# Optimization experiments

Hardware: AMD Instinct MI355X
Metric: run time of the kernel (lower is better)

Reference implementation:

```python
import jax, jax.numpy as jnp
import numpy as np

N, F, E = 2048, 512, 32  # batch, n_features (attention length), embedding_dim


def setup_inputs() -> dict:
    key = jax.random.key(0)
    ks = jax.random.split(key, 8)
    xav = np.sqrt(2.0 / (F + E))  # xavier_normal std for [F, E] params
    X = jax.random.normal(ks[0], (N, F), dtype=jnp.float32)
    Xi = jax.random.randint(ks[1], (N,), 0, 2).astype(jnp.float32)
    idx = jax.random.randint(ks[2], (N,), 0, F)
    I = jax.nn.one_hot(idx, F, dtype=jnp.float32)  # one-hot feature selector
    S = (jax.random.uniform(ks[3], (N, F)) < 0.5).astype(jnp.float32)
    S = S.at[:, 0].set(1.0)  # guarantee non-empty context per row
    return {
        "X": X, "Xi": Xi, "I": I, "S": S,
        "xi_w": jax.random.normal(ks[4], (F, E), jnp.float32) * xav,
        "xi_b": jax.random.normal(ks[5], (F, E), jnp.float32) * xav,
        "xs_w": jax.random.normal(ks[6], (F, E), jnp.float32) * xav,
        "xs_b": jax.random.normal(ks[7], (F, E), jnp.float32) * xav,
    }


def stable_softmax(x):
    # softmax along last dim; rows that are entirely -inf produce zeros
    m = jnp.max(x, axis=-1, keepdims=True)
    m = jnp.where(jnp.isfinite(m), m, jnp.zeros_like(m))
    e = jnp.exp(x - m)
    s = jnp.sum(e, axis=-1, keepdims=True)
    return e / jnp.maximum(s, jnp.asarray(1e-9, x.dtype))


def reference(X, Xi, I, S, xi_w, xi_b, xs_w, xs_b):
    # --- map_xs (attention aggregator) ---
    # FX: [N, F, E]; note the original reuses xs_featurizer_bias for the I-term
    FX = X[:, :, None] * xs_w[None] + xs_b[None] + (I @ xs_b)[:, None, :]
    keep = (S[:, :, None] * S[:, None, :]) > 0  # [N, F, F]
    mask = jnp.where(keep, 0.0, -jnp.inf).astype(FX.dtype)
    scale = jnp.asarray(1.0 / np.sqrt(E), FX.dtype)
    scores = mask + jnp.einsum('nqe,nke->nqk', FX * scale, FX)
    attn = stable_softmax(scores)  # [N, F, F]
    Fxs = jnp.einsum('nqk,nke->nqe', attn, FX).sum(axis=1) / S.sum(axis=1)[:, None]  # [N, E]
    # --- map_xi ---
    Iw = I @ xi_w  # [N, E]
    Ib = I @ xi_b  # [N, E]
    Fxi = Xi[:, None] * Iw + Ib
    # --- score / logz / logprob (binary, exp score) ---
    ulogp = jnp.log(jnp.exp(jnp.sum(Fxi * Fxs, axis=-1)))
    s0 = jnp.exp(jnp.sum(Ib * Fxs, axis=-1))          # Xi = 0
    s1 = jnp.exp(jnp.sum((Iw + Ib) * Fxs, axis=-1))   # Xi = 1
    logz = jnp.log(s0 + s1)
    return ulogp - logz  # [N]
```

## Files before the change

### kernel.cpp

```cpp
#include <hip/hip_runtime.h>
#include <math.h>

#define FF 512
#define EE 32
#define RS 40
#define FCAP 416
#define NTCAP 26

typedef __attribute__((ext_vector_type(8))) short bf16x8;
typedef __attribute__((ext_vector_type(4))) float f32x4;

#define SFOLD 0.5050092f

__device__ __forceinline__ unsigned short f2bf(float x) {
    unsigned int u = __float_as_uint(x);
    return (unsigned short)((u + 0x7fffu + ((u >> 16) & 1u)) >> 16);
}
__device__ __forceinline__ float bf2f(unsigned short h) {
    return __uint_as_float(((unsigned int)h) << 16);
}
__device__ __forceinline__ float esum4(f32x4 d) {
    return (__builtin_amdgcn_exp2f(d[0]) + __builtin_amdgcn_exp2f(d[1])) +
           (__builtin_amdgcn_exp2f(d[2]) + __builtin_amdgcn_exp2f(d[3]));
}

template <int NC>
__device__ __forceinline__ void pass1_cols(const unsigned short* __restrict__ myrow,
                                           float* __restrict__ Zs,
                                           int c0, int nt, int cnt, float pad, int lane) {
    bf16x8 bf[NC];
#pragma unroll
    for (int c = 0; c < NC; ++c)
        bf[c] = *(const bf16x8*)(myrow + (size_t)(c0 + c) * 16 * RS);
    float zA[NC], zB[NC];
#pragma unroll
    for (int c = 0; c < NC; ++c) { zA[c] = 0.f; zB[c] = 0.f; }
    const unsigned short* ap = myrow;
    int i = 0;
    for (; i + 2 <= nt; i += 2) {
        bf16x8 a0 = *(const bf16x8*)(ap);
        bf16x8 a1 = *(const bf16x8*)(ap + 16 * RS);
        ap += 32 * RS;
#pragma unroll
        for (int c = 0; c < NC; ++c) {
            f32x4 d0 = {0.f, 0.f, 0.f, 0.f};
            f32x4 d1 = {0.f, 0.f, 0.f, 0.f};
            d0 = __builtin_amdgcn_mfma_f32_16x16x32_bf16(a0, bf[c], d0, 0, 0, 0);
            d1 = __builtin_amdgcn_mfma_f32_16x16x32_bf16(a1, bf[c], d1, 0, 0, 0);
            zA[c] += esum4(d0);
            zB[c] += esum4(d1);
        }
    }
    if (i < nt) {
        bf16x8 a0 = *(const bf16x8*)(ap);
#pragma unroll
        for (int c = 0; c < NC; ++c) {
            f32x4 d0 = {0.f, 0.f, 0.f, 0.f};
            d0 = __builtin_amdgcn_mfma_f32_16x16x32_bf16(a0, bf[c], d0, 0, 0, 0);
            zA[c] += esum4(d0);
        }
    }
#pragma unroll
    for (int c = 0; c < NC; ++c) {
        float z = zA[c] + zB[c];
        z += __shfl_xor(z, 16);
        z += __shfl_xor(z, 32);
        if (lane < 16) {
            int q = (c0 + c) * 16 + lane;
            Zs[q] = (q < cnt) ? 1.f / fmaxf(z - pad, 1e-9f) : 0.f;
        }
    }
}

template <int NC>
__device__ __forceinline__ void pass2_cols(const unsigned short* __restrict__ myrow,
                                           const float* __restrict__ Zs,
                                           float* __restrict__ ws,
                                           int c0, int nt, int lane, int grp) {
    bf16x8 bf[NC];
#pragma unroll
    for (int c = 0; c < NC; ++c)
        bf[c] = *(const bf16x8*)(myrow + (size_t)(c0 + c) * 16 * RS);
    float wA[NC], wB[NC];
#pragma unroll
    for (int c = 0; c < NC; ++c) { wA[c] = 0.f; wB[c] = 0.f; }
    const unsigned short* ap = myrow;
    const float* zp = Zs + grp * 4;
    int i = 0;
    for (; i + 2 <= nt; i += 2) {
        bf16x8 a0 = *(const bf16x8*)(ap);
        bf16x8 a1 = *(const bf16x8*)(ap + 16 * RS);
        ap += 32 * RS;
        float4 z0 = *(const float4*)(zp);
        float4 z1 = *(const float4*)(zp + 16);
        zp += 32;
#pragma unroll
        for (int c = 0; c < NC; ++c) {
            f32x4 d0 = {0.f, 0.f, 0.f, 0.f};
            f32x4 d1 = {0.f, 0.f, 0.f, 0.f};
            d0 = __builtin_amdgcn_mfma_f32_16x16x32_bf16(a0, bf[c], d0, 0, 0, 0);
            d1 = __builtin_amdgcn_mfma_f32_16x16x32_bf16(a1, bf[c], d1, 0, 0, 0);
            float a = wA[c], b = wB[c];
            a = fmaf(__builtin_amdgcn_exp2f(d0[0]), z0.x, a);
            a = fmaf(__builtin_amdgcn_exp2f(d0[1]), z0.y, a);
            a = fmaf(__builtin_amdgcn_exp2f(d0[2]), z0.z, a);
            a = fmaf(__builtin_amdgcn_exp2f(d0[3]), z0.w, a);
            b = fmaf(__builtin_amdgcn_exp2f(d1[0]), z1.x, b);
            b = fmaf(__builtin_amdgcn_exp2f(d1[1]), z1.y, b);
            b = fmaf(__builtin_amdgcn_exp2f(d1[2]), z1.z, b);
            b = fmaf(__builtin_amdgcn_exp2f(d1[3]), z1.w, b);
            wA[c] = a; wB[c] = b;
        }
    }
    if (i < nt) {
        bf16x8 a0 = *(const bf16x8*)(ap);
        float4 z0 = *(const float4*)(zp);
#pragma unroll
        for (int c = 0; c < NC; ++c) {
            f32x4 d0 = {0.f, 0.f, 0.f, 0.f};
            d0 = __builtin_amdgcn_mfma_f32_16x16x32_bf16(a0, bf[c], d0, 0, 0, 0);
            float a = wA[c];
            a = fmaf(__builtin_amdgcn_exp2f(d0[0]), z0.x, a);
            a = fmaf(__builtin_amdgcn_exp2f(d0[1]), z0.y, a);
            a = fmaf(__builtin_amdgcn_exp2f(d0[2]), z0.z, a);
            a = fmaf(__builtin_amdgcn_exp2f(d0[3]), z0.w, a);
            wA[c] = a;
        }
    }
#pragma unroll
    for (int c = 0; c < NC; ++c) {
        float w = wA[c] + wB[c];
        w += __shfl_xor(w, 16);
        w += __shfl_xor(w, 32);
        if (lane < 16) ws[(c0 + c) * 16 + lane] = w;
    }
}

extern "C" __global__ void __launch_bounds__(512, 8)
model_kernel(const float* __restrict__ X, const float* __restrict__ Xi,
             const float* __restrict__ I, const float* __restrict__ S,
             const float* __restrict__ xi_w, const float* __restrict__ xi_b,
             const float* __restrict__ xs_w, const float* __restrict__ xs_b,
             float* __restrict__ out) {
    const int n = blockIdx.x;
    const int tid = threadIdx.x;
    const int lane = tid & 63;
    const int wv = tid >> 6;
    const int l15 = lane & 15;
    const int grp = lane >> 4;

    __shared__ __align__(16) unsigned short fxb[FCAP * RS];
    __shared__ unsigned short lst[FF];
    __shared__ __align__(16) float Zs[FCAP];
    __shared__ float ws[FCAP];
    __shared__ __align__(16) float idxb[EE];
    __shared__ float pf[16][EE];
    __shared__ float fxs_sh[EE];
    __shared__ int sh_idx;
    __shared__ int wbase[8];

    const float* Srow = S + (size_t)n * FF;
    const float* Irow = I + (size_t)n * FF;
    const float* Xrow = X + (size_t)n * FF;

    if (Irow[tid] > 0.5f) sh_idx = tid;
    bool act = Srow[tid] > 0.f;
    unsigned long long m = __ballot(act);
    int nb = __popcll(m & ((1ull << lane) - 1ull));
    if (lane == 0) wbase[wv] = __popcll(m);
    __syncthreads();

    int off = 0;
    for (int i = 0; i < wv; ++i) off += wbase[i];
    if (act) lst[off + nb] = (unsigned short)tid;
    int cntr = 0;
#pragma unroll
    for (int i = 0; i < 8; ++i) cntr += wbase[i];
    const int cnt = (cntr < FCAP) ? cntr : FCAP;
    int nt0 = (cnt + 15) >> 4;
    const int nt = (nt0 < NTCAP) ? nt0 : NTCAP;
    const int ntp16 = nt * 16;
    const int jend = ((nt + 1) >> 1) * 32;
    const int idx = sh_idx;
    if (tid < EE) idxb[tid] = xs_b[idx * EE + tid];
    __syncthreads();

    for (int jb = 0; jb < jend; jb += 64) {
        int j = jb + (tid >> 3);
        int e4 = (tid & 7) * 4;
        if (j < jend) {
            unsigned short h0 = 0, h1 = 0, h2 = 0, h3 = 0;
            if (j < cnt) {
                int f = lst[j];
                float xv = Xrow[f];
                float4 w4 = *(const float4*)(xs_w + f * EE + e4);
                float4 b4 = *(const float4*)(xs_b + f * EE + e4);
                float4 i4 = *(const float4*)(idxb + e4);
                h0 = f2bf(SFOLD * fmaf(xv, w4.x, b4.x + i4.x));
                h1 = f2bf(SFOLD * fmaf(xv, w4.y, b4.y + i4.y));
                h2 = f2bf(SFOLD * fmaf(xv, w4.z, b4.z + i4.z));
                h3 = f2bf(SFOLD * fmaf(xv, w4.w, b4.w + i4.w));
            }
            ushort4 pk = make_ushort4(h0, h1, h2, h3);
            *(ushort4*)(fxb + j * RS + e4) = pk;
        }
    }
    __syncthreads();

    const unsigned short* myrow = fxb + (size_t)l15 * RS + grp * 8;
    const float pad = (float)(ntp16 - cnt);

    const int cbase = nt >> 3, crem = nt & 7;
    const int ncols = cbase + (wv < crem ? 1 : 0);
    const int c0 = wv * cbase + (wv < crem ? wv : crem);

    switch (ncols) {
        case 1: pass1_cols<1>(myrow, Zs, c0, nt, cnt, pad, lane); break;
        case 2: pass1_cols<2>(myrow, Zs, c0, nt, cnt, pad, lane); break;
        case 3: pass1_cols<3>(myrow, Zs, c0, nt, cnt, pad, lane); break;
        case 4: pass1_cols<4>(myrow, Zs, c0, nt, cnt, pad, lane); break;
        default: break;
    }
    __syncthreads();

    switch (ncols) {
        case 1: pass2_cols<1>(myrow, Zs, ws, c0, nt, lane, grp); break;
        case 2: pass2_cols<2>(myrow, Zs, ws, c0, nt, lane, grp); break;
        case 3: pass2_cols<3>(myrow, Zs, ws, c0, nt, lane, grp); break;
        case 4: pass2_cols<4>(myrow, Zs, ws, c0, nt, lane, grp); break;
        default: break;
    }
    __syncthreads();

    {
        int e = tid & 31, g = tid >> 5;
        float acc = 0.f;
        for (int k = g; k < cnt; k += 16)
            acc += ws[k] * bf2f(fxb[k * RS + e]);
        pf[g][e] = acc;
    }
    __syncthreads();
    if (tid < EE) {
        float s = 0.f;
#pragma unroll
        for (int g = 0; g < 16; ++g) s += pf[g][tid];
        fxs_sh[tid] = s * (1.0f / SFOLD) / (float)cnt;
    }
    __syncthreads();
    if (tid < EE) {
        float fv = fxs_sh[tid];
        pf[0][tid] = xi_w[idx * EE + tid] * fv;
    }
    __syncthreads();
    if (tid == 0) {
        float a = 0.f;
#pragma unroll
        for (int e = 0; e < EE; ++e) a += pf[0][e];
        float xiv = Xi[n];
        float mm = fmaxf(a, 0.f);
        float sp = mm + logf(__expf(a - mm) + __expf(-mm));
        out[n] = xiv * a - sp;
    }
}

extern "C" void kernel_launch(void* const* d_in, const int* in_sizes, int n_in,
                              void* d_out, int out_size, void* d_ws, size_t ws_size,
                              hipStream_t stream) {
    const float* X    = (const float*)d_in[0];
    const float* Xi   = (const float*)d_in[1];
    const float* I    = (const float*)d_in[2];
    const float* S    = (const float*)d_in[3];
    const float* xi_w = (const float*)d_in[4];
    const float* xi_b = (const float*)d_in[5];
    const float* xs_w = (const float*)d_in[6];
    const float* xs_b = (const float*)d_in[7];
    float* out = (float*)d_out;
    const int N = in_sizes[1];
    hipLaunchKernelGGL(model_kernel, dim3(N), dim3(512), 0, stream,
                       X, Xi, I, S, xi_w, xi_b, xs_w, xs_b, out);
}
```

Measured before the change: 116.0 us.

## Split remainder column tiles across all waves to balance attention passes

When the number of 16-row tiles is 17 or 18, each wave takes two column tiles and the one or two leftover columns are split by row-pair ranges across all eight waves. Partial softmax denominators and weights are combined with shared-memory atomics, and the leftover denominators are inverted after a barrier. This removes the imbalance where a single wave handled a third column and set the critical path. It costs an extra barrier, atomics, and extra registers for the split-column operands.

```diff
diff --git a/kernel.cpp b/kernel.cpp
--- a/kernel.cpp
+++ b/kernel.cpp
@@ -23,21 +23,40 @@
     return (__builtin_amdgcn_exp2f(d[0]) + __builtin_amdgcn_exp2f(d[1])) +
            (__builtin_amdgcn_exp2f(d[2]) + __builtin_amdgcn_exp2f(d[3]));
 }
-
-template <int NC>
-__device__ __forceinline__ void pass1_cols(const unsigned short* __restrict__ myrow,
-                                           float* __restrict__ Zs,
-                                           int c0, int nt, int cnt, float pad, int lane) {
+__device__ __forceinline__ float wsum4(f32x4 d, float4 z, float acc) {
+    acc = fmaf(__builtin_amdgcn_exp2f(d[0]), z.x, acc);
+    acc = fmaf(__builtin_amdgcn_exp2f(d[1]), z.y, acc);
+    acc = fmaf(__builtin_amdgcn_exp2f(d[2]), z.z, acc);
+    acc = fmaf(__builtin_amdgcn_exp2f(d[3]), z.w, acc);
+    return acc;
+}
+
+template <int NC, int R>
+__device__ __forceinline__ void pass1_t(const unsigned short* __restrict__ myrow,
+                                        float* __restrict__ Zs,
+                                        int c0, int nt, int cnt, float pad,
+                                        int lane, int wv) {
     bf16x8 bf[NC];
 #pragma unroll
     for (int c = 0; c < NC; ++c)
         bf[c] = *(const bf16x8*)(myrow + (size_t)(c0 + c) * 16 * RS);
+    bf16x8 bs[R > 0 ? R : 1];
+    float sA[R > 0 ? R : 1], sB[R > 0 ? R : 1];
+    if (R > 0) {
+#pragma unroll
+        for (int s = 0; s < R; ++s) {
+            bs[s] = *(const bf16x8*)(myrow + (size_t)(nt - R + s) * 16 * RS);
+            sA[s] = 0.f; sB[s] = 0.f;
+        }
+    }
     float zA[NC], zB[NC];
 #pragma unroll
     for (int c = 0; c < NC; ++c) { zA[c] = 0.f; zB[c] = 0.f; }
+    const int NPf = nt >> 1;
+    const int NP = NPf + (nt & 1);
+    const int plo = (wv * NP) >> 3, phi = ((wv + 1) * NP) >> 3;
     const unsigned short* ap = myrow;
-    int i = 0;
-    for (; i + 2 <= nt; i += 2) {
+    for (int p = 0; p < NPf; ++p) {
         bf16x8 a0 = *(const bf16x8*)(ap);
         bf16x8 a1 = *(const bf16x8*)(ap + 16 * RS);
         ap += 32 * RS;
@@ -50,14 +69,33 @@
             zA[c] += esum4(d0);
             zB[c] += esum4(d1);
         }
-    }
-    if (i < nt) {
+        if (R > 0 && p >= plo && p < phi) {
+#pragma unroll
+            for (int s = 0; s < R; ++s) {
+                f32x4 d0 = {0.f, 0.f, 0.f, 0.f};
+                f32x4 d1 = {0.f, 0.f, 0.f, 0.f};
+                d0 = __builtin_amdgcn_mfma_f32_16x16x32_bf16(a0, bs[s], d0, 0, 0, 0);
+                d1 = __builtin_amdgcn_mfma_f32_16x16x32_bf16(a1, bs[s], d1, 0, 0, 0);
+                sA[s] += esum4(d0);
+                sB[s] += esum4(d1);
+            }
+        }
+    }
+    if (nt & 1) {
         bf16x8 a0 = *(const bf16x8*)(ap);
 #pragma unroll
         for (int c = 0; c < NC; ++c) {
             f32x4 d0 = {0.f, 0.f, 0.f, 0.f};
             d0 = __builtin_amdgcn_mfma_f32_16x16x32_bf16(a0, bf[c], d0, 0, 0, 0);
             zA[c] += esum4(d0);
+        }
+        if (R > 0 && NPf >= plo && NPf < phi) {
+#pragma unroll
+            for (int s = 0; s < R; ++s) {
+                f32x4 d0 = {0.f, 0.f, 0.f, 0.f};
+                d0 = __builtin_amdgcn_mfma_f32_16x16x32_bf16(a0, bs[s], d0, 0, 0, 0);
+                sA[s] += esum4(d0);
+            }
         }
     }
 #pragma unroll
@@ -70,24 +108,44 @@
             Zs[q] = (q < cnt) ? 1.f / fmaxf(z - pad, 1e-9f) : 0.f;
         }
     }
-}
-
-template <int NC>
-__device__ __forceinline__ void pass2_cols(const unsigned short* __restrict__ myrow,
-                                           const float* __restrict__ Zs,
-                                           float* __restrict__ ws,
-                                           int c0, int nt, int lane, int grp) {
+    if (R > 0) {
+#pragma unroll
+        for (int s = 0; s < R; ++s) {
+            float z = sA[s] + sB[s];
+            z += __shfl_xor(z, 16);
+            z += __shfl_xor(z, 32);
+            if (lane < 16) atomicAdd(&Zs[(nt - R + s) * 16 + lane], z);
+        }
+    }
+}
+
+template <int NC, int R>
+__device__ __forceinline__ void pass2_t(const unsigned short* __restrict__ myrow,
+                                        const float* __restrict__ Zs,
+                                        float* __restrict__ ws,
+                                        int c0, int nt, int lane, int grp, int wv) {
     bf16x8 bf[NC];
 #pragma unroll
     for (int c = 0; c < NC; ++c)
         bf[c] = *(const bf16x8*)(myrow + (size_t)(c0 + c) * 16 * RS);
+    bf16x8 bs[R > 0 ? R : 1];
+    float sA[R > 0 ? R : 1], sB[R > 0 ? R : 1];
+    if (R > 0) {
+#pragma unroll
+        for (int s = 0; s < R; ++s) {
+            bs[s] = *(const bf16x8*)(myrow + (size_t)(nt - R + s) * 16 * RS);
+            sA[s] = 0.f; sB[s] = 0.f;
+        }
+    }
     float wA[NC], wB[NC];
 #pragma unroll
     for (int c = 0; c < NC; ++c) { wA[c] = 0.f; wB[c] = 0.f; }
+    const int NPf = nt >> 1;
+    const int NP = NPf + (nt & 1);
+    const int plo = (wv * NP) >> 3, phi = ((wv + 1) * NP) >> 3;
     const unsigned short* ap = myrow;
     const float* zp = Zs + grp * 4;
-    int i = 0;
-    for (; i + 2 <= nt; i += 2) {
+    for (int p = 0; p < NPf; ++p) {
         bf16x8 a0 = *(const bf16x8*)(ap);
         bf16x8 a1 = *(const bf16x8*)(ap + 16 * RS);
         ap += 32 * RS;
@@ -100,31 +158,37 @@
             f32x4 d1 = {0.f, 0.f, 0.f, 0.f};
             d0 = __builtin_amdgcn_mfma_f32_16x16x32_bf16(a0, bf[c], d0, 0, 0, 0);
             d1 = __builtin_amdgcn_mfma_f32_16x16x32_bf16(a1, bf[c], d1, 0, 0, 0);
-            float a = wA[c], b = wB[c];
-            a = fmaf(__builtin_amdgcn_exp2f(d0[0]), z0.x, a);
-            a = fmaf(__builtin_amdgcn_exp2f(d0[1]), z0.y, a);
-            a = fmaf(__builtin_amdgcn_exp2f(d0[2]), z0.z, a);
-            a = fmaf(__builtin_amdgcn_exp2f(d0[3]), z0.w, a);
-            b = fmaf(__builtin_amdgcn_exp2f(d1[0]), z1.x, b);
-            b = fmaf(__builtin_amdgcn_exp2f(d1[1]), z1.y, b);
-            b = fmaf(__builtin_amdgcn_exp2f(d1[2]), z1.z, b);
-            b = fmaf(__builtin_amdgcn_exp2f(d1[3]), z1.w, b);
-            wA[c] = a; wB[c] = b;
-        }
-    }
-    if (i < nt) {
+            wA[c] = wsum4(d0, z0, wA[c]);
+            wB[c] = wsum4(d1, z1, wB[c]);
+        }
+        if (R > 0 && p >= plo && p < phi) {
+#pragma unroll
+            for (int s = 0; s < R; ++s) {
+                f32x4 d0 = {0.f, 0.f, 0.f, 0.f};
+                f32x4 d1 = {0.f, 0.f, 0.f, 0.f};
+                d0 = __builtin_amdgcn_mfma_f32_16x16x32_bf16(a0, bs[s], d0, 0, 0, 0);
+                d1 = __builtin_amdgcn_mfma_f32_16x16x32_bf16(a1, bs[s], d1, 0, 0, 0);
+                sA[s] = wsum4(d0, z0, sA[s]);
+                sB[s] = wsum4(d1, z1, sB[s]);
+            }
+        }
+    }
+    if (nt & 1) {
         bf16x8 a0 = *(const bf16x8*)(ap);
         float4 z0 = *(const float4*)(zp);
 #pragma unroll
         for (int c = 0; c < NC; ++c) {
             f32x4 d0 = {0.f, 0.f, 0.f, 0.f};
             d0 = __builtin_amdgcn_mfma_f32_16x16x32_bf16(a0, bf[c], d0, 0, 0, 0);
-            float a = wA[c];
-            a = fmaf(__builtin_amdgcn_exp2f(d0[0]), z0.x, a);
-            a = fmaf(__builtin_amdgcn_exp2f(d0[1]), z0.y, a);
-            a = fmaf(__builtin_amdgcn_exp2f(d0[2]), z0.z, a);
-            a = fmaf(__builtin_amdgcn_exp2f(d0[3]), z0.w, a);
-            wA[c] = a;
+            wA[c] = wsum4(d0, z0, wA[c]);
+        }
+        if (R > 0 && NPf >= plo && NPf < phi) {
+#pragma unroll
+            for (int s = 0; s < R; ++s) {
+                f32x4 d0 = {0.f, 0.f, 0.f, 0.f};
+                d0 = __builtin_amdgcn_mfma_f32_16x16x32_bf16(a0, bs[s], d0, 0, 0, 0);
+                sA[s] = wsum4(d0, z0, sA[s]);
+            }
         }
     }
 #pragma unroll
@@ -133,6 +197,15 @@
         w += __shfl_xor(w, 16);
         w += __shfl_xor(w, 32);
         if (lane < 16) ws[(c0 + c) * 16 + lane] = w;
+    }
+    if (R > 0) {
+#pragma unroll
+        for (int s = 0; s < R; ++s) {
+            float w = sA[s] + sB[s];
+            w += __shfl_xor(w, 16);
+            w += __shfl_xor(w, 32);
+            if (lane < 16) atomicAdd(&ws[(nt - R + s) * 16 + lane], w);
+        }
     }
 }
 
@@ -183,6 +256,13 @@
     const int jend = ((nt + 1) >> 1) * 32;
     const int idx = sh_idx;
     if (tid < EE) idxb[tid] = xs_b[idx * EE + tid];
+
+    const int r = (nt == 17) ? 1 : (nt == 18) ? 2 : 0;
+    if (r > 0 && tid < r * 16) {
+        int sq = (nt - r) * 16 + tid;
+        Zs[sq] = 0.f;
+        ws[sq] = 0.f;
+    }
     __syncthreads();
 
     for (int jb = 0; jb < jend; jb += 64) {
@@ -210,24 +290,38 @@
     const unsigned short* myrow = fxb + (size_t)l15 * RS + grp * 8;
     const float pad = (float)(ntp16 - cnt);
 
-    const int cbase = nt >> 3, crem = nt & 7;
-    const int ncols = cbase + (wv < crem ? 1 : 0);
-    const int c0 = wv * cbase + (wv < crem ? wv : crem);
-
-    switch (ncols) {
-        case 1: pass1_cols<1>(myrow, Zs, c0, nt, cnt, pad, lane); break;
-        case 2: pass1_cols<2>(myrow, Zs, c0, nt, cnt, pad, lane); break;
-        case 3: pass1_cols<3>(myrow, Zs, c0, nt, cnt, pad, lane); break;
-        case 4: pass1_cols<4>(myrow, Zs, c0, nt, cnt, pad, lane); break;
+    int ncols, c0;
+    if (r > 0) {
+        ncols = 2; c0 = wv * 2;
+    } else {
+        const int cbase = nt >> 3, crem = nt & 7;
+        ncols = cbase + (wv < crem ? 1 : 0);
+        c0 = wv * cbase + (wv < crem ? wv : crem);
+    }
+
+    if (r == 1)      pass1_t<2, 1>(myrow, Zs, c0, nt, cnt, pad, lane, wv);
+    else if (r == 2) pass1_t<2, 2>(myrow, Zs, c0, nt, cnt, pad, lane, wv);
+    else switch (ncols) {
+        case 1: pass1_t<1, 0>(myrow, Zs, c0, nt, cnt, pad, lane, wv); break;
+        case 2: pass1_t<2, 0>(myrow, Zs, c0, nt, cnt, pad, lane, wv); break;
+        case 3: pass1_t<3, 0>(myrow, Zs, c0, nt, cnt, pad, lane, wv); break;
+        case 4: pass1_t<4, 0>(myrow, Zs, c0, nt, cnt, pad, lane, wv); break;
         default: break;
     }
     __syncthreads();
-
-    switch (ncols) {
-        case 1: pass2_cols<1>(myrow, Zs, ws, c0, nt, lane, grp); break;
-        case 2: pass2_cols<2>(myrow, Zs, ws, c0, nt, lane, grp); break;
-        case 3: pass2_cols<3>(myrow, Zs, ws, c0, nt, lane, grp); break;
-        case 4: pass2_cols<4>(myrow, Zs, ws, c0, nt, lane, grp); break;
+    if (r > 0 && tid < r * 16) {
+        int q = (nt - r) * 16 + tid;
+        Zs[q] = (q < cnt) ? 1.f / fmaxf(Zs[q] - pad, 1e-9f) : 0.f;
+    }
+    __syncthreads();
+
+    if (r == 1)      pass2_t<2, 1>(myrow, Zs, ws, c0, nt, lane, grp, wv);
+    else if (r == 2) pass2_t<2, 2>(myrow, Zs, ws, c0, nt, lane, grp, wv);
+    else switch (ncols) {
+        case 1: pass2_t<1, 0>(myrow, Zs, ws, c0, nt, lane, grp, wv); break;
+        case 2: pass2_t<2, 0>(myrow, Zs, ws, c0, nt, lane, grp, wv); break;
+        case 3: pass2_t<3, 0>(myrow, Zs, ws, c0, nt, lane, grp, wv); break;
+        case 4: pass2_t<4, 0>(myrow, Zs, ws, c0, nt, lane, grp, wv); break;
         default: break;
     }
     __syncthreads();
```

New measurement: 337.3 us. +190.8%, slower.

## Split leftover column tiles across all waves when tile count is 17 or 18

Applied to the files above, without the earlier changes.

When the active-feature tile count is 17 or 18, each of the 8 waves now takes exactly 2 column tiles. The one or two leftover column tiles are split by row-pair ranges across all waves, and the partial softmax denominators and weighted sums are combined with shared-memory atomics. This targets load imbalance: with S at about 50% density the count lands near 256-288 features, so some waves would otherwise carry 3 columns while others carry 2. It adds an extra barrier, zero-initialisation, LDS atomics and a second code path for those cases.

```diff
diff --git a/kernel.cpp b/kernel.cpp
--- a/kernel.cpp
+++ b/kernel.cpp
@@ -22,6 +22,13 @@
 __device__ __forceinline__ float esum4(f32x4 d) {
     return (__builtin_amdgcn_exp2f(d[0]) + __builtin_amdgcn_exp2f(d[1])) +
            (__builtin_amdgcn_exp2f(d[2]) + __builtin_amdgcn_exp2f(d[3]));
+}
+__device__ __forceinline__ float wsum4(f32x4 d, float4 z, float acc) {
+    acc = fmaf(__builtin_amdgcn_exp2f(d[0]), z.x, acc);
+    acc = fmaf(__builtin_amdgcn_exp2f(d[1]), z.y, acc);
+    acc = fmaf(__builtin_amdgcn_exp2f(d[2]), z.z, acc);
+    acc = fmaf(__builtin_amdgcn_exp2f(d[3]), z.w, acc);
+    return acc;
 }
 
 template <int NC>
@@ -100,16 +107,8 @@
             f32x4 d1 = {0.f, 0.f, 0.f, 0.f};
             d0 = __builtin_amdgcn_mfma_f32_16x16x32_bf16(a0, bf[c], d0, 0, 0, 0);
             d1 = __builtin_amdgcn_mfma_f32_16x16x32_bf16(a1, bf[c], d1, 0, 0, 0);
-            float a = wA[c], b = wB[c];
-            a = fmaf(__builtin_amdgcn_exp2f(d0[0]), z0.x, a);
-            a = fmaf(__builtin_amdgcn_exp2f(d0[1]), z0.y, a);
-            a = fmaf(__builtin_amdgcn_exp2f(d0[2]), z0.z, a);
-            a = fmaf(__builtin_amdgcn_exp2f(d0[3]), z0.w, a);
-            b = fmaf(__builtin_amdgcn_exp2f(d1[0]), z1.x, b);
-            b = fmaf(__builtin_amdgcn_exp2f(d1[1]), z1.y, b);
-            b = fmaf(__builtin_amdgcn_exp2f(d1[2]), z1.z, b);
-            b = fmaf(__builtin_amdgcn_exp2f(d1[3]), z1.w, b);
-            wA[c] = a; wB[c] = b;
+            wA[c] = wsum4(d0, z0, wA[c]);
+            wB[c] = wsum4(d1, z1, wB[c]);
         }
     }
     if (i < nt) {
@@ -119,12 +118,7 @@
         for (int c = 0; c < NC; ++c) {
             f32x4 d0 = {0.f, 0.f, 0.f, 0.f};
             d0 = __builtin_amdgcn_mfma_f32_16x16x32_bf16(a0, bf[c], d0, 0, 0, 0);
-            float a = wA[c];
-            a = fmaf(__builtin_amdgcn_exp2f(d0[0]), z0.x, a);
-            a = fmaf(__builtin_amdgcn_exp2f(d0[1]), z0.y, a);
-            a = fmaf(__builtin_amdgcn_exp2f(d0[2]), z0.z, a);
-            a = fmaf(__builtin_amdgcn_exp2f(d0[3]), z0.w, a);
-            wA[c] = a;
+            wA[c] = wsum4(d0, z0, wA[c]);
         }
     }
 #pragma unroll
@@ -183,6 +177,13 @@
     const int jend = ((nt + 1) >> 1) * 32;
     const int idx = sh_idx;
     if (tid < EE) idxb[tid] = xs_b[idx * EE + tid];
+
+    const int r = (nt == 17 || nt == 18) ? (nt - 16) : 0;
+    if (r > 0 && tid < r * 16) {
+        int sq = 256 + tid;
+        Zs[sq] = 0.f;
+        ws[sq] = 0.f;
+    }
     __syncthreads();
 
     for (int jb = 0; jb < jend; jb += 64) {
@@ -210,9 +211,17 @@
     const unsigned short* myrow = fxb + (size_t)l15 * RS + grp * 8;
     const float pad = (float)(ntp16 - cnt);
 
-    const int cbase = nt >> 3, crem = nt & 7;
-    const int ncols = cbase + (wv < crem ? 1 : 0);
-    const int c0 = wv * cbase + (wv < crem ? wv : crem);
+    int ncols, c0;
+    if (r > 0) { ncols = 2; c0 = wv * 2; }
+    else {
+        const int cbase = nt >> 3, crem = nt & 7;
+        ncols = cbase + (wv < crem ? 1 : 0);
+        c0 = wv * cbase + (wv < crem ? wv : crem);
+    }
+
+    const int NPf = nt >> 1;
+    const int NP = NPf + (nt & 1);
+    const int plo = (wv * NP) >> 3, phi = ((wv + 1) * NP) >> 3;
 
     switch (ncols) {
         case 1: pass1_cols<1>(myrow, Zs, c0, nt, cnt, pad, lane); break;
@@ -221,6 +230,36 @@
         case 4: pass1_cols<4>(myrow, Zs, c0, nt, cnt, pad, lane); break;
         default: break;
     }
+    if (r > 0) {
+#pragma unroll
+        for (int s = 0; s < 2; ++s) {
+            if (s >= r) break;
+            bf16x8 bcol = *(const bf16x8*)(myrow + (size_t)(16 + s) * 16 * RS);
+            float accA = 0.f, accB = 0.f;
+            for (int p = plo; p < phi; ++p) {
+                const unsigned short* ap = myrow + (size_t)p * 32 * RS;
+                bf16x8 a0 = *(const bf16x8*)(ap);
+                f32x4 d0 = {0.f, 0.f, 0.f, 0.f};
+                d0 = __builtin_amdgcn_mfma_f32_16x16x32_bf16(a0, bcol, d0, 0, 0, 0);
+                accA += esum4(d0);
+                if (p < NPf) {
+                    bf16x8 a1 = *(const bf16x8*)(ap + 16 * RS);
+                    f32x4 d1 = {0.f, 0.f, 0.f, 0.f};
+                    d1 = __builtin_amdgcn_mfma_f32_16x16x32_bf16(a1, bcol, d1, 0, 0, 0);
+                    accB += esum4(d1);
+                }
+            }
+            float z = accA + accB;
+            z += __shfl_xor(z, 16);
+            z += __shfl_xor(z, 32);
+            if (lane < 16) atomicAdd(&Zs[(16 + s) * 16 + lane], z);
+        }
+    }
+    __syncthreads();
+    if (r > 0 && tid < r * 16) {
+        int q = 256 + tid;
+        Zs[q] = (q < cnt) ? 1.f / fmaxf(Zs[q] - pad, 1e-9f) : 0.f;
+    }
     __syncthreads();
 
     switch (ncols) {
@@ -229,6 +268,34 @@
         case 3: pass2_cols<3>(myrow, Zs, ws, c0, nt, lane, grp); break;
         case 4: pass2_cols<4>(myrow, Zs, ws, c0, nt, lane, grp); break;
         default: break;
+    }
+    if (r > 0) {
+#pragma unroll
+        for (int s = 0; s < 2; ++s) {
+            if (s >= r) break;
+            bf16x8 bcol = *(const bf16x8*)(myrow + (size_t)(16 + s) * 16 * RS);
+            float accA = 0.f, accB = 0.f;
+            for (int p = plo; p < phi; ++p) {
+                const unsigned short* ap = myrow + (size_t)p * 32 * RS;
+                const float* zp = Zs + p * 32 + grp * 4;
+                bf16x8 a0 = *(const bf16x8*)(ap);
+                float4 z0 = *(const float4*)(zp);
+                f32x4 d0 = {0.f, 0.f, 0.f, 0.f};
+                d0 = __builtin_amdgcn_mfma_f32_16x16x32_bf16(a0, bcol, d0, 0, 0, 0);
+                accA = wsum4(d0, z0, accA);
+                if (p < NPf) {
+                    bf16x8 a1 = *(const bf16x8*)(ap + 16 * RS);
+                    float4 z1 = *(const float4*)(zp + 16);
+                    f32x4 d1 = {0.f, 0.f, 0.f, 0.f};
+                    d1 = __builtin_amdgcn_mfma_f32_16x16x32_bf16(a1, bcol, d1, 0, 0, 0);
+                    accB = wsum4(d1, z1, accB);
+                }
+            }
+            float w = accA + accB;
+            w += __shfl_xor(w, 16);
+            w += __shfl_xor(w, 32);
+            if (lane < 16) atomicAdd(&ws[(16 + s) * 16 + lane], w);
+        }
     }
     __syncthreads();
 
```

Measured after the change: 117.6 us. Within noise of the previous version (+1.4%).

## Fuse softmax normalizer and weighted sum into one pass via projected values

Applied to the files above, without the earlier changes.

Since only the dot product of Fxs with xi_w is needed, each key's value is projected onto xi_w up front (g_k = FX_k·iw). A single MFMA pass then accumulates both the softmax denominator and the g-weighted numerator per query, and the per-query ratios are summed with an LDS atomic. This removes the second score recomputation pass, the per-embedding weighted reduction and several barriers, at the cost of doing extra FMAs in the one remaining pass and using a shared-memory atomic. The 4-column case is split into two 2-column calls, probably to limit register pressure.

```diff
diff --git a/kernel.cpp b/kernel.cpp
--- a/kernel.cpp
+++ b/kernel.cpp
@@ -16,123 +16,72 @@
     unsigned int u = __float_as_uint(x);
     return (unsigned short)((u + 0x7fffu + ((u >> 16) & 1u)) >> 16);
 }
-__device__ __forceinline__ float bf2f(unsigned short h) {
-    return __uint_as_float(((unsigned int)h) << 16);
-}
-__device__ __forceinline__ float esum4(f32x4 d) {
-    return (__builtin_amdgcn_exp2f(d[0]) + __builtin_amdgcn_exp2f(d[1])) +
-           (__builtin_amdgcn_exp2f(d[2]) + __builtin_amdgcn_exp2f(d[3]));
+
+__device__ __forceinline__ void zh4(f32x4 d, float4 g, float& z, float& h) {
+    float e0 = __builtin_amdgcn_exp2f(d[0]);
+    float e1 = __builtin_amdgcn_exp2f(d[1]);
+    float e2 = __builtin_amdgcn_exp2f(d[2]);
+    float e3 = __builtin_amdgcn_exp2f(d[3]);
+    z += (e0 + e1) + (e2 + e3);
+    h = fmaf(e0, g.x, fmaf(e1, g.y, fmaf(e2, g.z, fmaf(e3, g.w, h))));
 }
 
 template <int NC>
-__device__ __forceinline__ void pass1_cols(const unsigned short* __restrict__ myrow,
-                                           float* __restrict__ Zs,
-                                           int c0, int nt, int cnt, float pad, int lane) {
+__device__ __forceinline__ void fused_cols(const unsigned short* __restrict__ myrow,
+                                           const float* __restrict__ gs,
+                                           float* __restrict__ a_sh,
+                                           int c0, int nt, int cnt, float pad,
+                                           int lane, int grp) {
     bf16x8 bf[NC];
 #pragma unroll
     for (int c = 0; c < NC; ++c)
         bf[c] = *(const bf16x8*)(myrow + (size_t)(c0 + c) * 16 * RS);
-    float zA[NC], zB[NC];
-#pragma unroll
-    for (int c = 0; c < NC; ++c) { zA[c] = 0.f; zB[c] = 0.f; }
+    float zA[NC], zB[NC], hA[NC], hB[NC];
+#pragma unroll
+    for (int c = 0; c < NC; ++c) { zA[c] = 0.f; zB[c] = 0.f; hA[c] = 0.f; hB[c] = 0.f; }
     const unsigned short* ap = myrow;
+    const float* gp = gs + grp * 4;
     int i = 0;
     for (; i + 2 <= nt; i += 2) {
         bf16x8 a0 = *(const bf16x8*)(ap);
         bf16x8 a1 = *(const bf16x8*)(ap + 16 * RS);
         ap += 32 * RS;
+        float4 g0 = *(const float4*)(gp);
+        float4 g1 = *(const float4*)(gp + 16);
+        gp += 32;
 #pragma unroll
         for (int c = 0; c < NC; ++c) {
             f32x4 d0 = {0.f, 0.f, 0.f, 0.f};
             f32x4 d1 = {0.f, 0.f, 0.f, 0.f};
             d0 = __builtin_amdgcn_mfma_f32_16x16x32_bf16(a0, bf[c], d0, 0, 0, 0);
             d1 = __builtin_amdgcn_mfma_f32_16x16x32_bf16(a1, bf[c], d1, 0, 0, 0);
-            zA[c] += esum4(d0);
-            zB[c] += esum4(d1);
+            zh4(d0, g0, zA[c], hA[c]);
+            zh4(d1, g1, zB[c], hB[c]);
         }
     }
     if (i < nt) {
         bf16x8 a0 = *(const bf16x8*)(ap);
+        float4 g0 = *(const float4*)(gp);
 #pragma unroll
         for (int c = 0; c < NC; ++c) {
             f32x4 d0 = {0.f, 0.f, 0.f, 0.f};
             d0 = __builtin_amdgcn_mfma_f32_16x16x32_bf16(a0, bf[c], d0, 0, 0, 0);
-            zA[c] += esum4(d0);
+            zh4(d0, g0, zA[c], hA[c]);
         }
     }
 #pragma unroll
     for (int c = 0; c < NC; ++c) {
         float z = zA[c] + zB[c];
-        z += __shfl_xor(z, 16);
-        z += __shfl_xor(z, 32);
-        if (lane < 16) {
-            int q = (c0 + c) * 16 + lane;
-            Zs[q] = (q < cnt) ? 1.f / fmaxf(z - pad, 1e-9f) : 0.f;
-        }
-    }
-}
-
-template <int NC>
-__device__ __forceinline__ void pass2_cols(const unsigned short* __restrict__ myrow,
-                                           const float* __restrict__ Zs,
-                                           float* __restrict__ ws,
-                                           int c0, int nt, int lane, int grp) {
-    bf16x8 bf[NC];
-#pragma unroll
-    for (int c = 0; c < NC; ++c)
-        bf[c] = *(const bf16x8*)(myrow + (size_t)(c0 + c) * 16 * RS);
-    float wA[NC], wB[NC];
-#pragma unroll
-    for (int c = 0; c < NC; ++c) { wA[c] = 0.f; wB[c] = 0.f; }
-    const unsigned short* ap = myrow;
-    const float* zp = Zs + grp * 4;
-    int i = 0;
-    for (; i + 2 <= nt; i += 2) {
-        bf16x8 a0 = *(const bf16x8*)(ap);
-        bf16x8 a1 = *(const bf16x8*)(ap + 16 * RS);
-        ap += 32 * RS;
-        float4 z0 = *(const float4*)(zp);
-        float4 z1 = *(const float4*)(zp + 16);
-        zp += 32;
-#pragma unroll
-        for (int c = 0; c < NC; ++c) {
-            f32x4 d0 = {0.f, 0.f, 0.f, 0.f};
-            f32x4 d1 = {0.f, 0.f, 0.f, 0.f};
-            d0 = __builtin_amdgcn_mfma_f32_16x16x32_bf16(a0, bf[c], d0, 0, 0, 0);
-            d1 = __builtin_amdgcn_mfma_f32_16x16x32_bf16(a1, bf[c], d1, 0, 0, 0);
-            float a = wA[c], b = wB[c];
-            a = fmaf(__builtin_amdgcn_exp2f(d0[0]), z0.x, a);
-            a = fmaf(__builtin_amdgcn_exp2f(d0[1]), z0.y, a);
-            a = fmaf(__builtin_amdgcn_exp2f(d0[2]), z0.z, a);
-            a = fmaf(__builtin_amdgcn_exp2f(d0[3]), z0.w, a);
-            b = fmaf(__builtin_amdgcn_exp2f(d1[0]), z1.x, b);
-            b = fmaf(__builtin_amdgcn_exp2f(d1[1]), z1.y, b);
-            b = fmaf(__builtin_amdgcn_exp2f(d1[2]), z1.z, b);
-            b = fmaf(__builtin_amdgcn_exp2f(d1[3]), z1.w, b);
-            wA[c] = a; wB[c] = b;
-        }
-    }
-    if (i < nt) {
-        bf16x8 a0 = *(const bf16x8*)(ap);
-        float4 z0 = *(const float4*)(zp);
-#pragma unroll
-        for (int c = 0; c < NC; ++c) {
-            f32x4 d0 = {0.f, 0.f, 0.f, 0.f};
-            d0 = __builtin_amdgcn_mfma_f32_16x16x32_bf16(a0, bf[c], d0, 0, 0, 0);
-            float a = wA[c];
-            a = fmaf(__builtin_amdgcn_exp2f(d0[0]), z0.x, a);
-            a = fmaf(__builtin_amdgcn_exp2f(d0[1]), z0.y, a);
-            a = fmaf(__builtin_amdgcn_exp2f(d0[2]), z0.z, a);
-            a = fmaf(__builtin_amdgcn_exp2f(d0[3]), z0.w, a);
-            wA[c] = a;
-        }
-    }
-#pragma unroll
-    for (int c = 0; c < NC; ++c) {
-        float w = wA[c] + wB[c];
-        w += __shfl_xor(w, 16);
-        w += __shfl_xor(w, 32);
-        if (lane < 16) ws[(c0 + c) * 16 + lane] = w;
+        float h = hA[c] + hB[c];
+        z += __shfl_xor(z, 16); z += __shfl_xor(z, 32);
+        h += __shfl_xor(h, 16); h += __shfl_xor(h, 32);
+        int q = (c0 + c) * 16 + lane;
+        float val = (lane < 16 && q < cnt) ? h / fmaxf(z - pad, 1e-9f) : 0.f;
+        val += __shfl_xor(val, 1);
+        val += __shfl_xor(val, 2);
+        val += __shfl_xor(val, 4);
+        val += __shfl_xor(val, 8);
+        if (lane == 0) atomicAdd(a_sh, val);
     }
 }
 
@@ -151,11 +100,10 @@
 
     __shared__ __align__(16) unsigned short fxb[FCAP * RS];
     __shared__ unsigned short lst[FF];
-    __shared__ __align__(16) float Zs[FCAP];
-    __shared__ float ws[FCAP];
+    __shared__ __align__(16) float gs[FCAP];
     __shared__ __align__(16) float idxb[EE];
-    __shared__ float pf[16][EE];
-    __shared__ float fxs_sh[EE];
+    __shared__ __align__(16) float iw_sh[EE];
+    __shared__ float a_sh;
     __shared__ int sh_idx;
     __shared__ int wbase[8];
 
@@ -182,12 +130,17 @@
     const int ntp16 = nt * 16;
     const int jend = ((nt + 1) >> 1) * 32;
     const int idx = sh_idx;
-    if (tid < EE) idxb[tid] = xs_b[idx * EE + tid];
+    if (tid < EE) {
+        idxb[tid] = xs_b[idx * EE + tid];
+        iw_sh[tid] = xi_w[idx * EE + tid];
+    }
+    if (tid == 0) a_sh = 0.f;
     __syncthreads();
 
     for (int jb = 0; jb < jend; jb += 64) {
         int j = jb + (tid >> 3);
         int e4 = (tid & 7) * 4;
+        float part = 0.f;
         if (j < jend) {
             unsigned short h0 = 0, h1 = 0, h2 = 0, h3 = 0;
             if (j < cnt) {
@@ -196,14 +149,21 @@
                 float4 w4 = *(const float4*)(xs_w + f * EE + e4);
                 float4 b4 = *(const float4*)(xs_b + f * EE + e4);
                 float4 i4 = *(const float4*)(idxb + e4);
-                h0 = f2bf(SFOLD * fmaf(xv, w4.x, b4.x + i4.x));
-                h1 = f2bf(SFOLD * fmaf(xv, w4.y, b4.y + i4.y));
-                h2 = f2bf(SFOLD * fmaf(xv, w4.z, b4.z + i4.z));
-                h3 = f2bf(SFOLD * fmaf(xv, w4.w, b4.w + i4.w));
+                float r0 = SFOLD * fmaf(xv, w4.x, b4.x + i4.x);
+                float r1 = SFOLD * fmaf(xv, w4.y, b4.y + i4.y);
+                float r2 = SFOLD * fmaf(xv, w4.z, b4.z + i4.z);
+                float r3 = SFOLD * fmaf(xv, w4.w, b4.w + i4.w);
+                h0 = f2bf(r0); h1 = f2bf(r1); h2 = f2bf(r2); h3 = f2bf(r3);
+                const float* iw = iw_sh + e4;
+                part = fmaf(r0, iw[0], fmaf(r1, iw[1], fmaf(r2, iw[2], r3 * iw[3])));
             }
             ushort4 pk = make_ushort4(h0, h1, h2, h3);
             *(ushort4*)(fxb + j * RS + e4) = pk;
         }
+        part += __shfl_xor(part, 1);
+        part += __shfl_xor(part, 2);
+        part += __shfl_xor(part, 4);
+        if ((tid & 7) == 0 && j < jend) gs[j] = part;
     }
     __syncthreads();
 
@@ -215,47 +175,17 @@
     const int c0 = wv * cbase + (wv < crem ? wv : crem);
 
     switch (ncols) {
-        case 1: pass1_cols<1>(myrow, Zs, c0, nt, cnt, pad, lane); break;
-        case 2: pass1_cols<2>(myrow, Zs, c0, nt, cnt, pad, lane); break;
-        case 3: pass1_cols<3>(myrow, Zs, c0, nt, cnt, pad, lane); break;
-        case 4: pass1_cols<4>(myrow, Zs, c0, nt, cnt, pad, lane); break;
+        case 1: fused_cols<1>(myrow, gs, &a_sh, c0, nt, cnt, pad, lane, grp); break;
+        case 2: fused_cols<2>(myrow, gs, &a_sh, c0, nt, cnt, pad, lane, grp); break;
+        case 3: fused_cols<3>(myrow, gs, &a_sh, c0, nt, cnt, pad, lane, grp); break;
+        case 4: fused_cols<2>(myrow, gs, &a_sh, c0, nt, cnt, pad, lane, grp);
+                fused_cols<2>(myrow, gs, &a_sh, c0 + 2, nt, cnt, pad, lane, grp); break;
         default: break;
     }
     __syncthreads();
 
-    switch (ncols) {
-        case 1: pass2_cols<1>(myrow, Zs, ws, c0, nt, lane, grp); break;
-        case 2: pass2_cols<2>(myrow, Zs, ws, c0, nt, lane, grp); break;
-        case 3: pass2_cols<3>(myrow, Zs, ws, c0, nt, lane, grp); break;
-        case 4: pass2_cols<4>(myrow, Zs, ws, c0, nt, lane, grp); break;
-        default: break;
-    }
-    __syncthreads();
-
-    {
-        int e = tid & 31, g = tid >> 5;
-        float acc = 0.f;
-        for (int k = g; k < cnt; k += 16)
-            acc += ws[k] * bf2f(fxb[k * RS + e]);
-        pf[g][e] = acc;
-    }
-    __syncthreads();
-    if (tid < EE) {
-        float s = 0.f;
-#pragma unroll
-        for (int g = 0; g < 16; ++g) s += pf[g][tid];
-        fxs_sh[tid] = s * (1.0f / SFOLD) / (float)cnt;
-    }
-    __syncthreads();
-    if (tid < EE) {
-        float fv = fxs_sh[tid];
-        pf[0][tid] = xi_w[idx * EE + tid] * fv;
-    }
-    __syncthreads();
     if (tid == 0) {
-        float a = 0.f;
-#pragma unroll
-        for (int e = 0; e < EE; ++e) a += pf[0][e];
+        float a = a_sh / ((float)cnt * SFOLD);
         float xiv = Xi[n];
         float mm = fmaxf(a, 0.f);
         float sp = mm + logf(__expf(a - mm) + __expf(-mm));
```

Result: faster. 102.4 us (-11.8%).
